# Performance work log

Hardware: AMD Instinct MI355X
Metric: run time of the kernel (lower is better)

The kernel has to match this reference:

```python
import jax, jax.numpy as jnp
import numpy as np


def setup_inputs() -> dict:
    key = jax.random.key(0)
    k1, k2 = jax.random.split(key)
    token_inputs = jax.random.normal(k1, (4, 2048, 4096), dtype=jnp.float32)
    w_gate = jax.random.normal(k2, (4096, 64), dtype=jnp.float32)
    return {"token_inputs": token_inputs, "w_gate": w_gate, "expert_capacity": 40}


def reference(token_inputs, w_gate, expert_capacity):
    # Gating: [b, n, d] @ [d, e] -> [b, n, e]
    router_logits = jnp.einsum('bnd,de->bne', token_inputs, w_gate)

    # Router z-loss: mean of squared logsumexp over experts.
    z_loss = jnp.mean(jax.nn.logsumexp(router_logits, axis=-1) ** 2)

    router_probs = jax.nn.softmax(router_logits, axis=-1)
    num_experts = router_probs.shape[-1]

    # Top-1 (Switch) routing.
    expert_index = jnp.argmax(router_probs, axis=-1)          # [b, n]
    expert_gate = jnp.max(router_probs, axis=-1)              # [b, n]
    expert_mask = jax.nn.one_hot(expert_index, num_experts,
                                 dtype=router_probs.dtype)    # [b, n, e]

    # Load-balancing auxiliary loss.
    density = jnp.mean(expert_mask, axis=1)                   # [b, e] dispatch fraction
    density_proxy = jnp.mean(router_probs, axis=1)            # [b, e] mean prob
    aux_loss = jnp.mean(density * density_proxy) * (num_experts ** 2)

    # Capacity assignment via cumulative sum over tokens (0-based slot index).
    position_in_expert = (jnp.cumsum(expert_mask, axis=1) - 1.0) * expert_mask  # [b, n, e]
    within_capacity = (position_in_expert < expert_capacity).astype(router_probs.dtype) * expert_mask

    pos_idx = position_in_expert.astype(jnp.int32)            # [b, n, e]
    # Dispatch: one-hot over capacity slots, zeroed for dropped tokens. [b, n, e, c]
    dispatch_tensor = within_capacity[..., None] * jax.nn.one_hot(
        pos_idx, expert_capacity, dtype=router_probs.dtype)
    # Combine: dispatch scaled by the router gate probability.
    combine_tensor = dispatch_tensor * expert_gate[:, :, None, None]

    return dispatch_tensor, combine_tensor, aux_loss, z_loss
```

## Files before the change

kernel.cpp:

```cpp
#include <hip/hip_runtime.h>
#include <stdint.h>

#define B_    4
#define N_    2048
#define D_    4096
#define E_    64
#define TOKENS (B_ * N_)
#define KT    32
#define TM    64
#define KS    8
#define KCHUNK (D_ / KS)

typedef float vfloat4 __attribute__((ext_vector_type(4)));

__global__ __launch_bounds__(256) void k_gemm_z(const float* __restrict__ A,
                                                const float* __restrict__ W,
                                                float* __restrict__ P,
                                                float* __restrict__ out,
                                                float* __restrict__ probsum,
                                                float* __restrict__ losses) {
    __shared__ float As[KT][TM + 4];
    __shared__ float Ws[KT][E_ + 4];

    const int tid   = threadIdx.x;
    const int tok0  = blockIdx.x * TM;
    const int kc    = blockIdx.y;
    const int kbase = kc * KCHUNK;
    const int blin  = kc * gridDim.x + blockIdx.x;

    const int t0 = (tid >> 4) * 4;
    const int e0 = (tid & 15) * 4;

    const int a_kf = (tid & 7) * 4;
    const int a_t  = tid >> 3;
    const int w_e  = (tid & 15) * 4;
    const int w_k  = tid >> 4;

    vfloat4* zbase = reinterpret_cast<vfloat4*>(out) + (size_t)blin * 10240 + tid;
    int zstep = 0;
    const vfloat4 z4 = {0.f, 0.f, 0.f, 0.f};

    if (blin == 0) {
        if (tid < B_ * E_) probsum[tid] = 0.f;
        if (tid < 2)       losses[tid]  = 0.f;
    }

    float acc[4][4] = {{0.f}};

    #pragma unroll 1
    for (int kt = 0; kt < KCHUNK; kt += KT) {
        const float* gA = A + (size_t)tok0 * D_ + (size_t)(kbase + kt);
        #pragma unroll
        for (int it = 0; it < 2; ++it) {
            const int tok = a_t + it * 32;
            const float4 v = *reinterpret_cast<const float4*>(
                gA + (size_t)tok * D_ + a_kf);
            As[a_kf + 0][tok] = v.x;
            As[a_kf + 1][tok] = v.y;
            As[a_kf + 2][tok] = v.z;
            As[a_kf + 3][tok] = v.w;
        }
        const float* gW = W + (size_t)(kbase + kt) * E_;
        #pragma unroll
        for (int it = 0; it < 2; ++it) {
            const int kk = w_k + it * 16;
            const float4 v = *reinterpret_cast<const float4*>(gW + kk * E_ + w_e);
            *reinterpret_cast<float4*>(&Ws[kk][w_e]) = v;
        }
        __syncthreads();

        {
            const int nz = (kt < 8 * KT) ? 3 : 2;
            for (int j = 0; j < nz; ++j) {
                __builtin_nontemporal_store(z4, zbase + (size_t)zstep * 256);
                ++zstep;
            }
        }

        #pragma unroll
        for (int kk = 0; kk < KT; ++kk) {
            const float4 a = *reinterpret_cast<const float4*>(&As[kk][t0]);
            const float4 b = *reinterpret_cast<const float4*>(&Ws[kk][e0]);
            acc[0][0] += a.x * b.x; acc[0][1] += a.x * b.y;
            acc[0][2] += a.x * b.z; acc[0][3] += a.x * b.w;
            acc[1][0] += a.y * b.x; acc[1][1] += a.y * b.y;
            acc[1][2] += a.y * b.z; acc[1][3] += a.y * b.w;
            acc[2][0] += a.z * b.x; acc[2][1] += a.z * b.y;
            acc[2][2] += a.z * b.z; acc[2][3] += a.z * b.w;
            acc[3][0] += a.w * b.x; acc[3][1] += a.w * b.y;
            acc[3][2] += a.w * b.z; acc[3][3] += a.w * b.w;
        }
        __syncthreads();
    }

    float* base = P + ((size_t)kc * TOKENS + tok0) * E_;
    #pragma unroll
    for (int i = 0; i < 4; ++i) {
        const float4 v = make_float4(acc[i][0], acc[i][1], acc[i][2], acc[i][3]);
        *reinterpret_cast<float4*>(&base[(size_t)(t0 + i) * E_ + e0]) = v;
    }
}

__global__ __launch_bounds__(256) void k_softmax(const float* __restrict__ P,
                                                 int* __restrict__ idx,
                                                 float* __restrict__ gate,
                                                 float* __restrict__ probsum,
                                                 float* __restrict__ out_z) {
    const int tid  = threadIdx.x;
    const int wid  = tid >> 6;
    const int lane = tid & 63;
    const int tok  = blockIdx.x * 4 + wid;

    float l = 0.f;
    #pragma unroll
    for (int kc = 0; kc < KS; ++kc)
        l += P[((size_t)kc * TOKENS + tok) * E_ + lane];

    float m = l; int mi = lane;
    #pragma unroll
    for (int off = 32; off > 0; off >>= 1) {
        const float om = __shfl_down(m, off);
        const int   oi = __shfl_down(mi, off);
        if (om > m || (om == m && oi < mi)) { m = om; mi = oi; }
    }
    m  = __shfl(m, 0);
    mi = __shfl(mi, 0);

    const float p = __expf(l - m);
    float s = p;
    #pragma unroll
    for (int off = 32; off > 0; off >>= 1) s += __shfl_down(s, off);
    s = __shfl(s, 0);

    __shared__ float pacc[4][E_];
    __shared__ float zv[4];
    pacc[wid][lane] = p / s;
    if (lane == 0) {
        const float lse = m + logf(s);
        zv[wid]   = lse * lse;
        idx[tok]  = mi;
        gate[tok] = 1.0f / s;
    }
    __syncthreads();

    if (tid < E_) {
        const float ps = pacc[0][tid] + pacc[1][tid] + pacc[2][tid] + pacc[3][tid];
        const int b = (blockIdx.x * 4) / N_;
        atomicAdd(&probsum[b * E_ + tid], ps);
    }
    if (tid == 0)
        atomicAdd(out_z, (zv[0] + zv[1] + zv[2] + zv[3]) * (1.0f / (float)TOKENS));
}

__global__ __launch_bounds__(64) void k_posloss(const int* __restrict__ idx,
                                                const float* __restrict__ gate,
                                                const float* __restrict__ probsum,
                                                float* __restrict__ out,
                                                float* __restrict__ out_aux,
                                                int C, size_t half) {
    const int b = blockIdx.x >> 6;
    const int e = blockIdx.x & 63;
    const int lane = threadIdx.x;
    const int*   ib = idx  + b * N_;
    const float* gb = gate + b * N_;
    float* ob = out + (size_t)b * N_ * E_ * C;

    int running = 0;
    for (int step = 0; step < N_ / 64; ++step) {
        const int t = step * 64 + lane;
        const bool match = (ib[t] == e);
        const unsigned long long mask = __ballot(match);
        if (match) {
            const int p = running + __popcll(mask & ((1ull << lane) - 1ull));
            if (p < C) {
                const size_t off = (size_t)t * E_ * C + (size_t)e * C + p;
                ob[off] = 1.0f;
                ob[half + off] = gb[t];
            }
        }
        running += __popcll(mask);
    }
    if (lane == 0)
        atomicAdd(out_aux,
                  (float)running * probsum[b * E_ + e] * (1.0f / 262144.0f));
}

extern "C" void kernel_launch(void* const* d_in, const int* in_sizes, int n_in,
                              void* d_out, int out_size, void* d_ws, size_t ws_size,
                              hipStream_t stream) {
    const float* A = (const float*)d_in[0];
    const float* W = (const float*)d_in[1];
    float* out = (float*)d_out;

    const size_t half = ((size_t)out_size - 2) / 2;
    const int C = (int)(half / ((size_t)TOKENS * E_));

    float* P = (float*)d_ws;
    size_t off = (size_t)KS * TOKENS * E_;
    int*   idx     = (int*)(P + off);   off += TOKENS;
    float* gate    = P + off;           off += TOKENS;
    float* probsum = P + off;           off += B_ * E_;

    float* out_aux = out + 2 * half;
    float* out_z   = out + 2 * half + 1;

    k_gemm_z<<<dim3(TOKENS / TM, KS), 256, 0, stream>>>(A, W, P, out, probsum,
                                                        out_aux);
    k_softmax<<<TOKENS / 4, 256, 0, stream>>>(P, idx, gate, probsum, out_z);
    k_posloss<<<B_ * E_, 64, 0, stream>>>(idx, gate, probsum, out, out_aux, C, half);
}
```

Measured before the change: 336.4 us.

## Double-buffer GEMM tiles via direct global-to-LDS loads with 8x8 register tiles

Rewrites the gating GEMM so each 128-thread block computes a 128-token tile with an 8x8 per-thread register micro-tile. Operand tiles are copied straight from global memory into LDS with global_load_lds into two alternating buffers, so the next tile's load overlaps the current tile's compute, and the A tile uses an XOR swizzle to avoid bank conflicts. The aim is less LDS traffic per FMA, removal of the register-staged transpose, and hiding of load latency. In exchange, register pressure rises and there are half as many blocks, which may reduce occupancy. The zero-fill stores are redistributed to match the new grid.

```diff
diff --git a/kernel.cpp b/kernel.cpp
--- a/kernel.cpp
+++ b/kernel.cpp
@@ -7,97 +7,135 @@
 #define E_    64
 #define TOKENS (B_ * N_)
 #define KT    32
-#define TM    64
+#define TM    128
 #define KS    8
 #define KCHUNK (D_ / KS)
+#define NITER (KCHUNK / KT)
 
 typedef float vfloat4 __attribute__((ext_vector_type(4)));
 
-__global__ __launch_bounds__(256) void k_gemm_z(const float* __restrict__ A,
+#define GL2LDS16(g, s) __builtin_amdgcn_global_load_lds(                     \
+    (const __attribute__((address_space(1))) void*)(g),                      \
+    (__attribute__((address_space(3))) void*)(s), 16, 0, 0)
+
+__global__ __launch_bounds__(128) void k_gemm_z(const float* __restrict__ A,
                                                 const float* __restrict__ W,
                                                 float* __restrict__ P,
                                                 float* __restrict__ out,
                                                 float* __restrict__ probsum,
                                                 float* __restrict__ losses) {
-    __shared__ float As[KT][TM + 4];
-    __shared__ float Ws[KT][E_ + 4];
+    __shared__ float As[2][TM][KT];
+    __shared__ float Ws[2][KT][E_];
 
     const int tid   = threadIdx.x;
+    const int l     = tid & 63;
+    const int w     = tid >> 6;
     const int tok0  = blockIdx.x * TM;
     const int kc    = blockIdx.y;
     const int kbase = kc * KCHUNK;
     const int blin  = kc * gridDim.x + blockIdx.x;
 
-    const int t0 = (tid >> 4) * 4;
-    const int e0 = (tid & 15) * 4;
-
-    const int a_kf = (tid & 7) * 4;
-    const int a_t  = tid >> 3;
-    const int w_e  = (tid & 15) * 4;
-    const int w_k  = tid >> 4;
-
-    vfloat4* zbase = reinterpret_cast<vfloat4*>(out) + (size_t)blin * 10240 + tid;
-    int zstep = 0;
+    const int t0 = (tid >> 3) * 8;
+    const int e0 = (tid & 7) * 8;
+    const int sw = (tid >> 3) & 7;
+
+    const float* pA[8];
+    #pragma unroll
+    for (int q = 0; q < 8; ++q) {
+        const int i  = w * 8 + q;
+        const int tk = i * 8 + (l >> 3);
+        const int ks = (l & 7) ^ (i & 7);
+        pA[q] = A + (size_t)(tok0 + tk) * D_ + kbase + ks * 4;
+    }
+    const float* pW[4];
+    #pragma unroll
+    for (int q = 0; q < 4; ++q) {
+        const int i  = w * 4 + q;
+        const int kk = i * 4 + (l >> 4);
+        pW[q] = W + (size_t)(kbase + kk) * E_ + (l & 15) * 4;
+    }
+
+    vfloat4* zbase = reinterpret_cast<vfloat4*>(out) + (size_t)blin * 20480 + tid;
     const vfloat4 z4 = {0.f, 0.f, 0.f, 0.f};
 
     if (blin == 0) {
-        if (tid < B_ * E_) probsum[tid] = 0.f;
-        if (tid < 2)       losses[tid]  = 0.f;
-    }
-
-    float acc[4][4] = {{0.f}};
+        probsum[tid] = 0.f;
+        probsum[tid + 128] = 0.f;
+        if (tid < 2) losses[tid] = 0.f;
+    }
+
+    #pragma unroll
+    for (int q = 0; q < 8; ++q) {
+        GL2LDS16(pA[q], &As[0][(w * 8 + q) * 8][0]);
+        pA[q] += KT;
+    }
+    #pragma unroll
+    for (int q = 0; q < 4; ++q) {
+        GL2LDS16(pW[q], &Ws[0][(w * 4 + q) * 4][0]);
+        pW[q] += KT * E_;
+    }
+    __syncthreads();
+
+    float acc[8][8];
+    #pragma unroll
+    for (int i = 0; i < 8; ++i)
+        #pragma unroll
+        for (int j = 0; j < 8; ++j) acc[i][j] = 0.f;
 
     #pragma unroll 1
-    for (int kt = 0; kt < KCHUNK; kt += KT) {
-        const float* gA = A + (size_t)tok0 * D_ + (size_t)(kbase + kt);
+    for (int kt = 0; kt < NITER; ++kt) {
+        const int cur = kt & 1;
+        const int nxt = cur ^ 1;
+
+        if (kt + 1 < NITER) {
+            #pragma unroll
+            for (int q = 0; q < 8; ++q) {
+                GL2LDS16(pA[q], &As[nxt][(w * 8 + q) * 8][0]);
+                pA[q] += KT;
+            }
+            #pragma unroll
+            for (int q = 0; q < 4; ++q) {
+                GL2LDS16(pW[q], &Ws[nxt][(w * 4 + q) * 4][0]);
+                pW[q] += KT * E_;
+            }
+        }
+
         #pragma unroll
-        for (int it = 0; it < 2; ++it) {
-            const int tok = a_t + it * 32;
-            const float4 v = *reinterpret_cast<const float4*>(
-                gA + (size_t)tok * D_ + a_kf);
-            As[a_kf + 0][tok] = v.x;
-            As[a_kf + 1][tok] = v.y;
-            As[a_kf + 2][tok] = v.z;
-            As[a_kf + 3][tok] = v.w;
-        }
-        const float* gW = W + (size_t)(kbase + kt) * E_;
+        for (int j = 0; j < 10; ++j)
+            __builtin_nontemporal_store(z4, zbase + (size_t)(kt * 10 + j) * 128);
+
         #pragma unroll
-        for (int it = 0; it < 2; ++it) {
-            const int kk = w_k + it * 16;
-            const float4 v = *reinterpret_cast<const float4*>(gW + kk * E_ + w_e);
-            *reinterpret_cast<float4*>(&Ws[kk][w_e]) = v;
+        for (int kk4 = 0; kk4 < 8; ++kk4) {
+            float4 av[8];
+            const int so = ((kk4 ^ sw) << 2);
+            #pragma unroll
+            for (int i = 0; i < 8; ++i)
+                av[i] = *reinterpret_cast<const float4*>(&As[cur][t0 + i][so]);
+            #pragma unroll
+            for (int k = 0; k < 4; ++k) {
+                const float4 w0 = *reinterpret_cast<const float4*>(&Ws[cur][kk4 * 4 + k][e0]);
+                const float4 w1 = *reinterpret_cast<const float4*>(&Ws[cur][kk4 * 4 + k][e0 + 4]);
+                #pragma unroll
+                for (int i = 0; i < 8; ++i) {
+                    const float a = (k == 0) ? av[i].x : (k == 1) ? av[i].y
+                                  : (k == 2) ? av[i].z : av[i].w;
+                    acc[i][0] += a * w0.x; acc[i][1] += a * w0.y;
+                    acc[i][2] += a * w0.z; acc[i][3] += a * w0.w;
+                    acc[i][4] += a * w1.x; acc[i][5] += a * w1.y;
+                    acc[i][6] += a * w1.z; acc[i][7] += a * w1.w;
+                }
+            }
         }
         __syncthreads();
-
-        {
-            const int nz = (kt < 8 * KT) ? 3 : 2;
-            for (int j = 0; j < nz; ++j) {
-                __builtin_nontemporal_store(z4, zbase + (size_t)zstep * 256);
-                ++zstep;
-            }
-        }
-
-        #pragma unroll
-        for (int kk = 0; kk < KT; ++kk) {
-            const float4 a = *reinterpret_cast<const float4*>(&As[kk][t0]);
-            const float4 b = *reinterpret_cast<const float4*>(&Ws[kk][e0]);
-            acc[0][0] += a.x * b.x; acc[0][1] += a.x * b.y;
-            acc[0][2] += a.x * b.z; acc[0][3] += a.x * b.w;
-            acc[1][0] += a.y * b.x; acc[1][1] += a.y * b.y;
-            acc[1][2] += a.y * b.z; acc[1][3] += a.y * b.w;
-            acc[2][0] += a.z * b.x; acc[2][1] += a.z * b.y;
-            acc[2][2] += a.z * b.z; acc[2][3] += a.z * b.w;
-            acc[3][0] += a.w * b.x; acc[3][1] += a.w * b.y;
-            acc[3][2] += a.w * b.z; acc[3][3] += a.w * b.w;
-        }
-        __syncthreads();
     }
 
     float* base = P + ((size_t)kc * TOKENS + tok0) * E_;
     #pragma unroll
-    for (int i = 0; i < 4; ++i) {
-        const float4 v = make_float4(acc[i][0], acc[i][1], acc[i][2], acc[i][3]);
-        *reinterpret_cast<float4*>(&base[(size_t)(t0 + i) * E_ + e0]) = v;
+    for (int i = 0; i < 8; ++i) {
+        *reinterpret_cast<float4*>(&base[(size_t)(t0 + i) * E_ + e0]) =
+            make_float4(acc[i][0], acc[i][1], acc[i][2], acc[i][3]);
+        *reinterpret_cast<float4*>(&base[(size_t)(t0 + i) * E_ + e0 + 4]) =
+            make_float4(acc[i][4], acc[i][5], acc[i][6], acc[i][7]);
     }
 }
 
@@ -204,7 +242,7 @@
     float* out_aux = out + 2 * half;
     float* out_z   = out + 2 * half + 1;
 
-    k_gemm_z<<<dim3(TOKENS / TM, KS), 256, 0, stream>>>(A, W, P, out, probsum,
+    k_gemm_z<<<dim3(TOKENS / TM, KS), 128, 0, stream>>>(A, W, P, out, probsum,
                                                         out_aux);
     k_softmax<<<TOKENS / 4, 256, 0, stream>>>(P, idx, gate, probsum, out_z);
     k_posloss<<<B_ * E_, 64, 0, stream>>>(idx, gate, probsum, out, out_aux, C, half);
```

After: 337.0 us. About the same (+0.2%).
